# Performance work log

Measured on AMD Instinct MI355X. Metric: run time of the kernel, lower is better.

## Reference

```python
import jax, jax.numpy as jnp
import numpy as np

B, S, D, H, E, K = 8, 2048, 1024, 2048, 8, 2


def setup_inputs() -> dict:
    key = jax.random.key(0)
    k0, k1, k2, k3, k4 = jax.random.split(key, 5)
    x = jax.random.normal(k0, (B, S, D), jnp.float32)
    gate_w = jax.random.normal(k1, (E, D), jnp.float32) * (D ** -0.5)
    w1 = jax.random.normal(k2, (E, H, D), jnp.float32) * (D ** -0.5)
    w3 = jax.random.normal(k3, (E, H, D), jnp.float32) * (D ** -0.5)
    w2 = jax.random.normal(k4, (E, D, H), jnp.float32) * (H ** -0.5)
    return {"x": x, "gate_w": gate_w, "w1": w1, "w3": w3, "w2": w2, "k": K}


def reference(x, gate_w, w1, w3, w2, k):
    # Flatten tokens: [B, S, D] -> [T, D]
    x2 = x.reshape(-1, x.shape[-1])
    T = x2.shape[0]
    n_exp = gate_w.shape[0]
    # Gating: top-k logits, softmax over the k selected (in float32, cast back)
    logits = x2 @ gate_w.T                                  # [T, E]
    top_w, sel = jax.lax.top_k(logits, k)                   # [T, k] each
    top_w = jax.nn.softmax(top_w.astype(jnp.float32), axis=1).astype(x.dtype)
    # Dense combine weights [T, E]: zero for unselected experts (faithful to
    # the gather/scatter-add loop; topk indices are unique per token).
    cw = jnp.zeros((T, n_exp), x.dtype).at[jnp.arange(T)[:, None], sel].add(top_w)
    # Per-expert SwiGLU FFN, accumulated with combine weights.
    out = jnp.zeros_like(x2)
    for e in range(n_exp):  # fixed small structural loop over experts
        h = jax.nn.silu(x2 @ w1[e].T) * (x2 @ w3[e].T)      # [T, H]
        out = out + cw[:, e:e + 1] * (h @ w2[e].T)          # [T, D]
    return out.reshape(x.shape)
```

## Files before the change

kernel.cpp:

```cpp
#include <hip/hip_runtime.h>
#include <hip/hip_bf16.h>
#include <cstdint>


#define T_TOK 16384
#define DIM   1024
#define HID   2048
#define NEXP  8
#define MAX_TILES 264

typedef __bf16 bf16;
typedef bf16  bf16x8 __attribute__((ext_vector_type(8)));
typedef bf16  bf16x4 __attribute__((ext_vector_type(4)));
typedef float f32x16 __attribute__((ext_vector_type(16)));

__device__ __forceinline__ void async_cp16(const void* g, void* l) {
  __builtin_amdgcn_global_load_lds((const __attribute__((address_space(1))) void*)g,
                                   (__attribute__((address_space(3))) void*)l, 16, 0, 0);
}

__global__ __launch_bounds__(256) void zero_kernel(float4* __restrict__ out4, int n4,
                                                   int* __restrict__ ctrl) {
  const int i = blockIdx.x * 256 + threadIdx.x;
  if (i < n4) out4[i] = float4{0.f, 0.f, 0.f, 0.f};
  if (blockIdx.x == 0 && threadIdx.x < 64) ctrl[threadIdx.x] = 0;
}

__global__ __launch_bounds__(256) void cvt_kernel(const float* __restrict__ in,
                                                  bf16* __restrict__ out, int n4) {
  const int i = blockIdx.x * 256 + threadIdx.x;
  if (i < n4) {
    const float4 v = ((const float4*)in)[i];
    bf16x4 o;
    o[0] = (bf16)v.x; o[1] = (bf16)v.y; o[2] = (bf16)v.z; o[3] = (bf16)v.w;
    ((bf16x4*)out)[i] = o;
  }
}

__global__ __launch_bounds__(64) void gate_kernel(const float* __restrict__ x,
                                                  const float* __restrict__ gw,
                                                  int* __restrict__ sel,
                                                  float* __restrict__ selw) {
  const int t = blockIdx.x;
  const int lane = threadIdx.x;
  const float* xr = x + (size_t)t * DIM;
  float acc[NEXP];
#pragma unroll
  for (int e = 0; e < NEXP; e++) acc[e] = 0.f;
  for (int i = lane; i < DIM; i += 64) {
    const float xv = xr[i];
#pragma unroll
    for (int e = 0; e < NEXP; e++) acc[e] += xv * gw[e * DIM + i];
  }
#pragma unroll
  for (int e = 0; e < NEXP; e++) {
#pragma unroll
    for (int m = 1; m < 64; m <<= 1) acc[e] += __shfl_xor(acc[e], m);
  }
  if (lane == 0) {
    int e0 = 0; float l0 = acc[0];
#pragma unroll
    for (int e = 1; e < NEXP; e++) if (acc[e] > l0) { l0 = acc[e]; e0 = e; }
    int e1 = -1; float l1 = -3.4e38f;
#pragma unroll
    for (int e = 0; e < NEXP; e++) if (e != e0 && acc[e] > l1) { l1 = acc[e]; e1 = e; }
    const float ex = expf(l1 - l0);
    const float w0 = 1.f / (1.f + ex);
    sel[t * 2] = e0;  sel[t * 2 + 1] = e1;
    selw[t * 2] = w0; selw[t * 2 + 1] = 1.f - w0;
  }
}

__global__ __launch_bounds__(256) void count_kernel(const int* __restrict__ sel,
                                                    int* __restrict__ counts) {
  const int i = blockIdx.x * 256 + threadIdx.x;
  const int lane = threadIdx.x & 63;
  const int e = sel[i];
#pragma unroll
  for (int ee = 0; ee < NEXP; ee++) {
    const unsigned long long mask = __ballot(e == ee);
    if (e == ee) {
      const int leader = __ffsll(mask) - 1;
      if (lane == leader) atomicAdd(&counts[ee], __popcll(mask));
    }
  }
}

__global__ void tilemap_kernel(const int* __restrict__ counts, int* __restrict__ segoff,
                               int* __restrict__ tile_e, int* __restrict__ tile_m,
                               int* __restrict__ ntiles) {
  if (threadIdx.x == 0 && blockIdx.x == 0) {
    int off = 0, nt = 0;
    for (int e = 0; e < NEXP; e++) {
      segoff[e] = off;
      const int c = counts[e];
      for (int m = 0; m < c; m += 128) { tile_e[nt] = e; tile_m[nt] = m; nt++; }
      off += c;
    }
    segoff[NEXP] = off;
    ntiles[0] = nt;
  }
}

__global__ __launch_bounds__(256) void fill_kernel(const int* __restrict__ sel,
                                                   const float* __restrict__ selw,
                                                   const int* __restrict__ segoff,
                                                   int* __restrict__ fill,
                                                   int* __restrict__ tokl,
                                                   float* __restrict__ wl) {
  const int t = blockIdx.x * 256 + threadIdx.x;
  const int lane = threadIdx.x & 63;
#pragma unroll
  for (int s = 0; s < 2; s++) {
    const int e = sel[t * 2 + s];
    const float w = selw[t * 2 + s];
    for (int ee = 0; ee < NEXP; ee++) {
      const unsigned long long mask = __ballot(e == ee);
      if (e == ee) {
        const int leader = __ffsll(mask) - 1;
        const int cnt = __popcll(mask);
        int base = 0;
        if (lane == leader) base = atomicAdd(&fill[ee], cnt);
        base = __shfl(base, leader);
        const int pos = base + __popcll(mask & ((1ull << lane) - 1ull));
        const int idx = segoff[ee] + pos;
        tokl[idx] = t;
        wl[idx] = w;
      }
    }
  }
}

__global__ __launch_bounds__(256) void gemm_act_kernel(
    const bf16* __restrict__ xb, const bf16* __restrict__ w1b, const bf16* __restrict__ w3b,
    const int* __restrict__ tokl, const int* __restrict__ counts, const int* __restrict__ segoff,
    const int* __restrict__ tile_e, const int* __restrict__ tile_m, const int* __restrict__ ntiles,
    bf16* __restrict__ act) {
  const int tile = blockIdx.y;
  if (tile >= *ntiles) return;
  const int e   = tile_e[tile];
  const int m0  = tile_m[tile];
  const int n0  = blockIdx.x * 64;
  const int Ne  = counts[e];
  const int seg = segoff[e];

  __shared__ bf16 As[128 * 64];
  __shared__ bf16 Bs1[64 * 64];
  __shared__ bf16 Bs3[64 * 64];

  const int tid = threadIdx.x;
  const int lane = tid & 63;
  const int wv = tid >> 6;
  const int sr = tid >> 3;
  const int scb = (tid & 7) ^ (sr & 7);

  const bf16* aptr[4];
#pragma unroll
  for (int i = 0; i < 4; i++) {
    int m = m0 + sr + 32 * i; if (m > Ne - 1) m = Ne - 1;
    aptr[i] = xb + (size_t)tokl[seg + m] * DIM + scb * 8;
  }
  const bf16 *b1p[2], *b3p[2];
#pragma unroll
  for (int i = 0; i < 2; i++) {
    const int n = n0 + sr + 32 * i;
    b1p[i] = w1b + ((size_t)e * HID + n) * DIM + scb * 8;
    b3p[i] = w3b + ((size_t)e * HID + n) * DIM + scb * 8;
  }

  f32x16 acc1[2], acc3[2];
#pragma unroll
  for (int i = 0; i < 2; i++)
#pragma unroll
    for (int j = 0; j < 16; j++) { acc1[i][j] = 0.f; acc3[i][j] = 0.f; }

  const int lwm = (wv & 1) * 64;
  const int lwn = (wv >> 1) * 32;
  const int l31 = lane & 31;
  const int lhi = lane >> 5;
  const int l7  = l31 & 7;

  for (int k0 = 0; k0 < DIM; k0 += 64) {
#pragma unroll
    for (int i = 0; i < 4; i++)
      async_cp16(aptr[i] + k0, (char*)As + i * 4096 + tid * 16);
#pragma unroll
    for (int i = 0; i < 2; i++) {
      async_cp16(b1p[i] + k0, (char*)Bs1 + i * 4096 + tid * 16);
      async_cp16(b3p[i] + k0, (char*)Bs3 + i * 4096 + tid * 16);
    }
    __syncthreads();
#pragma unroll
    for (int ks = 0; ks < 4; ks++) {
      const int swz = (((ks * 2 + lhi) ^ l7) * 8);
      bf16x8 a0 = *(const bf16x8*)(As + (lwm + l31) * 64 + swz);
      bf16x8 a1 = *(const bf16x8*)(As + (lwm + 32 + l31) * 64 + swz);
      bf16x8 b1 = *(const bf16x8*)(Bs1 + (lwn + l31) * 64 + swz);
      bf16x8 b3 = *(const bf16x8*)(Bs3 + (lwn + l31) * 64 + swz);
      acc1[0] = __builtin_amdgcn_mfma_f32_32x32x16_bf16(a0, b1, acc1[0], 0, 0, 0);
      acc3[0] = __builtin_amdgcn_mfma_f32_32x32x16_bf16(a0, b3, acc3[0], 0, 0, 0);
      acc1[1] = __builtin_amdgcn_mfma_f32_32x32x16_bf16(a1, b1, acc1[1], 0, 0, 0);
      acc3[1] = __builtin_amdgcn_mfma_f32_32x32x16_bf16(a1, b3, acc3[1], 0, 0, 0);
    }
    __syncthreads();
  }

#pragma unroll
  for (int ms = 0; ms < 2; ms++) {
#pragma unroll
    for (int r = 0; r < 16; r++) {
      const int row = lwm + 32 * ms + (r & 3) + 8 * (r >> 2) + 4 * lhi;
      const int m = m0 + row;
      if (m < Ne) {
        const float h1 = acc1[ms][r];
        const float h3 = acc3[ms][r];
        const float sv = h1 / (1.f + __expf(-h1)) * h3;
        act[(size_t)(seg + m) * HID + (n0 + lwn + l31)] = (bf16)sv;
      }
    }
  }
}

__global__ __launch_bounds__(256) void gemm_out_kernel(
    const bf16* __restrict__ act, const bf16* __restrict__ w2b,
    const int* __restrict__ tokl, const float* __restrict__ wl,
    const int* __restrict__ counts, const int* __restrict__ segoff,
    const int* __restrict__ tile_e, const int* __restrict__ tile_m, const int* __restrict__ ntiles,
    float* __restrict__ out) {
  const int tile = blockIdx.y;
  if (tile >= *ntiles) return;
  const int e   = tile_e[tile];
  const int m0  = tile_m[tile];
  const int n0  = blockIdx.x * 128;
  const int Ne  = counts[e];
  const int seg = segoff[e];

  __shared__ bf16 As[128 * 64];
  __shared__ bf16 Bs[128 * 64];
  __shared__ int   sh_tok[128];
  __shared__ float sh_w[128];

  const int tid = threadIdx.x;
  const int lane = tid & 63;
  const int wv = tid >> 6;
  const int sr = tid >> 3;
  const int scb = (tid & 7) ^ (sr & 7);

  if (tid < 128) {
    const int m = m0 + tid;
    if (m < Ne) { sh_tok[tid] = tokl[seg + m]; sh_w[tid] = wl[seg + m]; }
    else        { sh_tok[tid] = -1;            sh_w[tid] = 0.f; }
  }

  const bf16* aptr[4];
#pragma unroll
  for (int i = 0; i < 4; i++) {
    int m = m0 + sr + 32 * i; if (m > Ne - 1) m = Ne - 1;
    aptr[i] = act + (size_t)(seg + m) * HID + scb * 8;
  }
  const bf16* bptr[4];
#pragma unroll
  for (int i = 0; i < 4; i++) {
    const int d = n0 + sr + 32 * i;
    bptr[i] = w2b + ((size_t)e * DIM + d) * HID + scb * 8;
  }

  f32x16 acc[4];
#pragma unroll
  for (int i = 0; i < 4; i++)
#pragma unroll
    for (int j = 0; j < 16; j++) acc[i][j] = 0.f;

  const int lwm = (wv & 1) * 64;
  const int lwn = (wv >> 1) * 64;
  const int l31 = lane & 31;
  const int lhi = lane >> 5;
  const int l7  = l31 & 7;

  for (int k0 = 0; k0 < HID; k0 += 64) {
#pragma unroll
    for (int i = 0; i < 4; i++)
      async_cp16(aptr[i] + k0, (char*)As + i * 4096 + tid * 16);
#pragma unroll
    for (int i = 0; i < 4; i++)
      async_cp16(bptr[i] + k0, (char*)Bs + i * 4096 + tid * 16);
    __syncthreads();
#pragma unroll
    for (int ks = 0; ks < 4; ks++) {
      const int swz = (((ks * 2 + lhi) ^ l7) * 8);
      bf16x8 a0 = *(const bf16x8*)(As + (lwm + l31) * 64 + swz);
      bf16x8 a1 = *(const bf16x8*)(As + (lwm + 32 + l31) * 64 + swz);
      bf16x8 b0 = *(const bf16x8*)(Bs + (lwn + l31) * 64 + swz);
      bf16x8 b1 = *(const bf16x8*)(Bs + (lwn + 32 + l31) * 64 + swz);
      acc[0] = __builtin_amdgcn_mfma_f32_32x32x16_bf16(a0, b0, acc[0], 0, 0, 0);
      acc[1] = __builtin_amdgcn_mfma_f32_32x32x16_bf16(a0, b1, acc[1], 0, 0, 0);
      acc[2] = __builtin_amdgcn_mfma_f32_32x32x16_bf16(a1, b0, acc[2], 0, 0, 0);
      acc[3] = __builtin_amdgcn_mfma_f32_32x32x16_bf16(a1, b1, acc[3], 0, 0, 0);
    }
    __syncthreads();
  }

#pragma unroll
  for (int mi = 0; mi < 2; mi++) {
#pragma unroll
    for (int ni = 0; ni < 2; ni++) {
#pragma unroll
      for (int r = 0; r < 16; r++) {
        const int row = lwm + 32 * mi + (r & 3) + 8 * (r >> 2) + 4 * lhi;
        const int tok = sh_tok[row];
        if (tok >= 0) {
          const int col = n0 + lwn + 32 * ni + l31;
          atomicAdd(&out[(size_t)tok * DIM + col], sh_w[row] * acc[mi * 2 + ni][r]);
        }
      }
    }
  }
}

extern "C" void kernel_launch(void* const* d_in, const int* in_sizes, int n_in,
                              void* d_out, int out_size, void* d_ws, size_t ws_size,
                              hipStream_t stream) {
  const float* x  = (const float*)d_in[0];
  const float* gw = (const float*)d_in[1];
  const float* w1 = (const float*)d_in[2];
  const float* w3 = (const float*)d_in[3];
  const float* w2 = (const float*)d_in[4];
  float* out = (float*)d_out;

  char* ws = (char*)d_ws;
  size_t off = 0;
  auto alloc = [&](size_t bytes) -> char* {
    char* p = ws + off; off += (bytes + 255) & ~(size_t)255; return p;
  };

  int* ctrl = (int*)alloc(4096);
  int* counts = ctrl;
  int* fill   = ctrl + 8;
  int* segoff = ctrl + 16;
  int* ntiles = ctrl + 32;
  int* tile_e = ctrl + 64;
  int* tile_m = ctrl + 512;
  int*   sel  = (int*)alloc((size_t)T_TOK * 2 * 4);
  float* selw = (float*)alloc((size_t)T_TOK * 2 * 4);
  int*   tokl = (int*)alloc((size_t)2 * T_TOK * 4);
  float* wl   = (float*)alloc((size_t)2 * T_TOK * 4);

  bf16* act  = (bf16*)alloc((size_t)2 * T_TOK * HID * 2);
  bf16* w1b  = (bf16*)alloc((size_t)NEXP * HID * DIM * 2);
  bf16* w3b  = (bf16*)alloc((size_t)NEXP * HID * DIM * 2);
  bf16* xb   = (bf16*)alloc((size_t)T_TOK * DIM * 2);
  bf16* w2b  = xb;
  (void)ws_size; (void)in_sizes; (void)n_in; (void)out_size;

  zero_kernel<<<T_TOK * DIM / 4 / 256, 256, 0, stream>>>((float4*)out, T_TOK * DIM / 4, ctrl);

  cvt_kernel<<<16384, 256, 0, stream>>>(x,  xb,  T_TOK * DIM / 4);
  cvt_kernel<<<16384, 256, 0, stream>>>(w1, w1b, NEXP * HID * DIM / 4);
  cvt_kernel<<<16384, 256, 0, stream>>>(w3, w3b, NEXP * HID * DIM / 4);

  gate_kernel<<<T_TOK, 64, 0, stream>>>(x, gw, sel, selw);
  count_kernel<<<2 * T_TOK / 256, 256, 0, stream>>>(sel, counts);
  tilemap_kernel<<<1, 64, 0, stream>>>(counts, segoff, tile_e, tile_m, ntiles);
  fill_kernel<<<T_TOK / 256, 256, 0, stream>>>(sel, selw, segoff, fill, tokl, wl);

  gemm_act_kernel<<<dim3(HID / 64, MAX_TILES), 256, 0, stream>>>(
      xb, w1b, w3b, tokl, counts, segoff, tile_e, tile_m, ntiles, act);

  cvt_kernel<<<16384, 256, 0, stream>>>(w2, w2b, NEXP * DIM * HID / 4);

  gemm_out_kernel<<<dim3(DIM / 128, MAX_TILES), 256, 0, stream>>>(
      act, w2b, tokl, wl, counts, segoff, tile_e, tile_m, ntiles, out);
}
```

Baseline: 1.036 ms.

## Enlarge GEMM tiles and replace atomic scatter-add with per-slot stores plus combine

Result: slower. 1.196 ms (+15.4%).

```diff
diff --git a/kernel.cpp b/kernel.cpp
--- a/kernel.cpp
+++ b/kernel.cpp
@@ -10,8 +10,10 @@
 #define MAX_TILES 264
 
 typedef __bf16 bf16;
+typedef _Float16 f16;
 typedef bf16  bf16x8 __attribute__((ext_vector_type(8)));
 typedef bf16  bf16x4 __attribute__((ext_vector_type(4)));
+typedef f16   f16x4  __attribute__((ext_vector_type(4)));
 typedef float f32x16 __attribute__((ext_vector_type(16)));
 
 __device__ __forceinline__ void async_cp16(const void* g, void* l) {
@@ -19,11 +21,8 @@
                                    (__attribute__((address_space(3))) void*)l, 16, 0, 0);
 }
 
-__global__ __launch_bounds__(256) void zero_kernel(float4* __restrict__ out4, int n4,
-                                                   int* __restrict__ ctrl) {
-  const int i = blockIdx.x * 256 + threadIdx.x;
-  if (i < n4) out4[i] = float4{0.f, 0.f, 0.f, 0.f};
-  if (blockIdx.x == 0 && threadIdx.x < 64) ctrl[threadIdx.x] = 0;
+__global__ void zero_ctrl_kernel(int* __restrict__ ctrl) {
+  if (threadIdx.x < 64) ctrl[threadIdx.x] = 0;
 }
 
 __global__ __launch_bounds__(256) void cvt_kernel(const float* __restrict__ in,
@@ -103,17 +102,14 @@
 }
 
 __global__ __launch_bounds__(256) void fill_kernel(const int* __restrict__ sel,
-                                                   const float* __restrict__ selw,
                                                    const int* __restrict__ segoff,
                                                    int* __restrict__ fill,
-                                                   int* __restrict__ tokl,
-                                                   float* __restrict__ wl) {
+                                                   int* __restrict__ tokl) {
   const int t = blockIdx.x * 256 + threadIdx.x;
   const int lane = threadIdx.x & 63;
 #pragma unroll
   for (int s = 0; s < 2; s++) {
     const int e = sel[t * 2 + s];
-    const float w = selw[t * 2 + s];
     for (int ee = 0; ee < NEXP; ee++) {
       const unsigned long long mask = __ballot(e == ee);
       if (e == ee) {
@@ -123,9 +119,7 @@
         if (lane == leader) base = atomicAdd(&fill[ee], cnt);
         base = __shfl(base, leader);
         const int pos = base + __popcll(mask & ((1ull << lane) - 1ull));
-        const int idx = segoff[ee] + pos;
-        tokl[idx] = t;
-        wl[idx] = w;
+        tokl[segoff[ee] + pos] = t | (s << 20);
       }
     }
   }
@@ -140,13 +134,13 @@
   if (tile >= *ntiles) return;
   const int e   = tile_e[tile];
   const int m0  = tile_m[tile];
-  const int n0  = blockIdx.x * 64;
+  const int n0  = blockIdx.x * 128;
   const int Ne  = counts[e];
   const int seg = segoff[e];
 
   __shared__ bf16 As[128 * 64];
-  __shared__ bf16 Bs1[64 * 64];
-  __shared__ bf16 Bs3[64 * 64];
+  __shared__ bf16 Bs1[128 * 64];
+  __shared__ bf16 Bs3[128 * 64];
 
   const int tid = threadIdx.x;
   const int lane = tid & 63;
@@ -158,24 +152,26 @@
 #pragma unroll
   for (int i = 0; i < 4; i++) {
     int m = m0 + sr + 32 * i; if (m > Ne - 1) m = Ne - 1;
-    aptr[i] = xb + (size_t)tokl[seg + m] * DIM + scb * 8;
-  }
-  const bf16 *b1p[2], *b3p[2];
-#pragma unroll
-  for (int i = 0; i < 2; i++) {
+    aptr[i] = xb + (size_t)(tokl[seg + m] & 0xFFFFF) * DIM + scb * 8;
+  }
+  const bf16 *b1p[4], *b3p[4];
+#pragma unroll
+  for (int i = 0; i < 4; i++) {
     const int n = n0 + sr + 32 * i;
     b1p[i] = w1b + ((size_t)e * HID + n) * DIM + scb * 8;
     b3p[i] = w3b + ((size_t)e * HID + n) * DIM + scb * 8;
   }
 
-  f32x16 acc1[2], acc3[2];
+  f32x16 acc1[2][2], acc3[2][2];
 #pragma unroll
   for (int i = 0; i < 2; i++)
 #pragma unroll
-    for (int j = 0; j < 16; j++) { acc1[i][j] = 0.f; acc3[i][j] = 0.f; }
+    for (int j = 0; j < 2; j++)
+#pragma unroll
+      for (int r = 0; r < 16; r++) { acc1[i][j][r] = 0.f; acc3[i][j][r] = 0.f; }
 
   const int lwm = (wv & 1) * 64;
-  const int lwn = (wv >> 1) * 32;
+  const int lwn = (wv >> 1) * 64;
   const int l31 = lane & 31;
   const int lhi = lane >> 5;
   const int l7  = l31 & 7;
@@ -185,22 +181,29 @@
     for (int i = 0; i < 4; i++)
       async_cp16(aptr[i] + k0, (char*)As + i * 4096 + tid * 16);
 #pragma unroll
-    for (int i = 0; i < 2; i++) {
+    for (int i = 0; i < 4; i++)
       async_cp16(b1p[i] + k0, (char*)Bs1 + i * 4096 + tid * 16);
+#pragma unroll
+    for (int i = 0; i < 4; i++)
       async_cp16(b3p[i] + k0, (char*)Bs3 + i * 4096 + tid * 16);
-    }
     __syncthreads();
 #pragma unroll
     for (int ks = 0; ks < 4; ks++) {
       const int swz = (((ks * 2 + lhi) ^ l7) * 8);
-      bf16x8 a0 = *(const bf16x8*)(As + (lwm + l31) * 64 + swz);
-      bf16x8 a1 = *(const bf16x8*)(As + (lwm + 32 + l31) * 64 + swz);
-      bf16x8 b1 = *(const bf16x8*)(Bs1 + (lwn + l31) * 64 + swz);
-      bf16x8 b3 = *(const bf16x8*)(Bs3 + (lwn + l31) * 64 + swz);
-      acc1[0] = __builtin_amdgcn_mfma_f32_32x32x16_bf16(a0, b1, acc1[0], 0, 0, 0);
-      acc3[0] = __builtin_amdgcn_mfma_f32_32x32x16_bf16(a0, b3, acc3[0], 0, 0, 0);
-      acc1[1] = __builtin_amdgcn_mfma_f32_32x32x16_bf16(a1, b1, acc1[1], 0, 0, 0);
-      acc3[1] = __builtin_amdgcn_mfma_f32_32x32x16_bf16(a1, b3, acc3[1], 0, 0, 0);
+      bf16x8 a0  = *(const bf16x8*)(As  + (lwm + l31) * 64 + swz);
+      bf16x8 a1  = *(const bf16x8*)(As  + (lwm + 32 + l31) * 64 + swz);
+      bf16x8 b10 = *(const bf16x8*)(Bs1 + (lwn + l31) * 64 + swz);
+      bf16x8 b11 = *(const bf16x8*)(Bs1 + (lwn + 32 + l31) * 64 + swz);
+      bf16x8 b30 = *(const bf16x8*)(Bs3 + (lwn + l31) * 64 + swz);
+      bf16x8 b31 = *(const bf16x8*)(Bs3 + (lwn + 32 + l31) * 64 + swz);
+      acc1[0][0] = __builtin_amdgcn_mfma_f32_32x32x16_bf16(a0, b10, acc1[0][0], 0, 0, 0);
+      acc1[0][1] = __builtin_amdgcn_mfma_f32_32x32x16_bf16(a0, b11, acc1[0][1], 0, 0, 0);
+      acc1[1][0] = __builtin_amdgcn_mfma_f32_32x32x16_bf16(a1, b10, acc1[1][0], 0, 0, 0);
+      acc1[1][1] = __builtin_amdgcn_mfma_f32_32x32x16_bf16(a1, b11, acc1[1][1], 0, 0, 0);
+      acc3[0][0] = __builtin_amdgcn_mfma_f32_32x32x16_bf16(a0, b30, acc3[0][0], 0, 0, 0);
+      acc3[0][1] = __builtin_amdgcn_mfma_f32_32x32x16_bf16(a0, b31, acc3[0][1], 0, 0, 0);
+      acc3[1][0] = __builtin_amdgcn_mfma_f32_32x32x16_bf16(a1, b30, acc3[1][0], 0, 0, 0);
+      acc3[1][1] = __builtin_amdgcn_mfma_f32_32x32x16_bf16(a1, b31, acc3[1][1], 0, 0, 0);
     }
     __syncthreads();
   }
@@ -212,10 +215,13 @@
       const int row = lwm + 32 * ms + (r & 3) + 8 * (r >> 2) + 4 * lhi;
       const int m = m0 + row;
       if (m < Ne) {
-        const float h1 = acc1[ms][r];
-        const float h3 = acc3[ms][r];
-        const float sv = h1 / (1.f + __expf(-h1)) * h3;
-        act[(size_t)(seg + m) * HID + (n0 + lwn + l31)] = (bf16)sv;
+        bf16* arow = act + (size_t)(seg + m) * HID + n0 + lwn;
+#pragma unroll
+        for (int ns = 0; ns < 2; ns++) {
+          const float h1 = acc1[ms][ns][r];
+          const float h3 = acc3[ms][ns][r];
+          arow[32 * ns + l31] = (bf16)(h1 / (1.f + __expf(-h1)) * h3);
+        }
       }
     }
   }
@@ -223,22 +229,21 @@
 
 __global__ __launch_bounds__(256) void gemm_out_kernel(
     const bf16* __restrict__ act, const bf16* __restrict__ w2b,
-    const int* __restrict__ tokl, const float* __restrict__ wl,
+    const int* __restrict__ tokl,
     const int* __restrict__ counts, const int* __restrict__ segoff,
     const int* __restrict__ tile_e, const int* __restrict__ tile_m, const int* __restrict__ ntiles,
-    float* __restrict__ out) {
+    f16* __restrict__ y) {
   const int tile = blockIdx.y;
   if (tile >= *ntiles) return;
   const int e   = tile_e[tile];
   const int m0  = tile_m[tile];
-  const int n0  = blockIdx.x * 128;
+  const int n0  = blockIdx.x * 256;
   const int Ne  = counts[e];
   const int seg = segoff[e];
 
   __shared__ bf16 As[128 * 64];
-  __shared__ bf16 Bs[128 * 64];
-  __shared__ int   sh_tok[128];
-  __shared__ float sh_w[128];
+  __shared__ bf16 Bs[256 * 64];
+  __shared__ int  sh_tok[128];
 
   const int tid = threadIdx.x;
   const int lane = tid & 63;
@@ -248,8 +253,7 @@
 
   if (tid < 128) {
     const int m = m0 + tid;
-    if (m < Ne) { sh_tok[tid] = tokl[seg + m]; sh_w[tid] = wl[seg + m]; }
-    else        { sh_tok[tid] = -1;            sh_w[tid] = 0.f; }
+    sh_tok[tid] = (m < Ne) ? tokl[seg + m] : -1;
   }
 
   const bf16* aptr[4];
@@ -258,21 +262,23 @@
     int m = m0 + sr + 32 * i; if (m > Ne - 1) m = Ne - 1;
     aptr[i] = act + (size_t)(seg + m) * HID + scb * 8;
   }
-  const bf16* bptr[4];
-#pragma unroll
-  for (int i = 0; i < 4; i++) {
+  const bf16* bptr[8];
+#pragma unroll
+  for (int i = 0; i < 8; i++) {
     const int d = n0 + sr + 32 * i;
     bptr[i] = w2b + ((size_t)e * DIM + d) * HID + scb * 8;
   }
 
-  f32x16 acc[4];
-#pragma unroll
-  for (int i = 0; i < 4; i++)
-#pragma unroll
-    for (int j = 0; j < 16; j++) acc[i][j] = 0.f;
+  f32x16 acc[2][4];
+#pragma unroll
+  for (int i = 0; i < 2; i++)
+#pragma unroll
+    for (int j = 0; j < 4; j++)
+#pragma unroll
+      for (int r = 0; r < 16; r++) acc[i][j][r] = 0.f;
 
   const int lwm = (wv & 1) * 64;
-  const int lwn = (wv >> 1) * 64;
+  const int lwn = (wv >> 1) * 128;
   const int l31 = lane & 31;
   const int lhi = lane >> 5;
   const int l7  = l31 & 7;
@@ -282,7 +288,7 @@
     for (int i = 0; i < 4; i++)
       async_cp16(aptr[i] + k0, (char*)As + i * 4096 + tid * 16);
 #pragma unroll
-    for (int i = 0; i < 4; i++)
+    for (int i = 0; i < 8; i++)
       async_cp16(bptr[i] + k0, (char*)Bs + i * 4096 + tid * 16);
     __syncthreads();
 #pragma unroll
@@ -292,10 +298,16 @@
       bf16x8 a1 = *(const bf16x8*)(As + (lwm + 32 + l31) * 64 + swz);
       bf16x8 b0 = *(const bf16x8*)(Bs + (lwn + l31) * 64 + swz);
       bf16x8 b1 = *(const bf16x8*)(Bs + (lwn + 32 + l31) * 64 + swz);
-      acc[0] = __builtin_amdgcn_mfma_f32_32x32x16_bf16(a0, b0, acc[0], 0, 0, 0);
-      acc[1] = __builtin_amdgcn_mfma_f32_32x32x16_bf16(a0, b1, acc[1], 0, 0, 0);
-      acc[2] = __builtin_amdgcn_mfma_f32_32x32x16_bf16(a1, b0, acc[2], 0, 0, 0);
-      acc[3] = __builtin_amdgcn_mfma_f32_32x32x16_bf16(a1, b1, acc[3], 0, 0, 0);
+      bf16x8 b2 = *(const bf16x8*)(Bs + (lwn + 64 + l31) * 64 + swz);
+      bf16x8 b3 = *(const bf16x8*)(Bs + (lwn + 96 + l31) * 64 + swz);
+      acc[0][0] = __builtin_amdgcn_mfma_f32_32x32x16_bf16(a0, b0, acc[0][0], 0, 0, 0);
+      acc[0][1] = __builtin_amdgcn_mfma_f32_32x32x16_bf16(a0, b1, acc[0][1], 0, 0, 0);
+      acc[0][2] = __builtin_amdgcn_mfma_f32_32x32x16_bf16(a0, b2, acc[0][2], 0, 0, 0);
+      acc[0][3] = __builtin_amdgcn_mfma_f32_32x32x16_bf16(a0, b3, acc[0][3], 0, 0, 0);
+      acc[1][0] = __builtin_amdgcn_mfma_f32_32x32x16_bf16(a1, b0, acc[1][0], 0, 0, 0);
+      acc[1][1] = __builtin_amdgcn_mfma_f32_32x32x16_bf16(a1, b1, acc[1][1], 0, 0, 0);
+      acc[1][2] = __builtin_amdgcn_mfma_f32_32x32x16_bf16(a1, b2, acc[1][2], 0, 0, 0);
+      acc[1][3] = __builtin_amdgcn_mfma_f32_32x32x16_bf16(a1, b3, acc[1][3], 0, 0, 0);
     }
     __syncthreads();
   }
@@ -303,18 +315,36 @@
 #pragma unroll
   for (int mi = 0; mi < 2; mi++) {
 #pragma unroll
-    for (int ni = 0; ni < 2; ni++) {
-#pragma unroll
-      for (int r = 0; r < 16; r++) {
-        const int row = lwm + 32 * mi + (r & 3) + 8 * (r >> 2) + 4 * lhi;
-        const int tok = sh_tok[row];
-        if (tok >= 0) {
-          const int col = n0 + lwn + 32 * ni + l31;
-          atomicAdd(&out[(size_t)tok * DIM + col], sh_w[row] * acc[mi * 2 + ni][r]);
-        }
+    for (int r = 0; r < 16; r++) {
+      const int row = lwm + 32 * mi + (r & 3) + 8 * (r >> 2) + 4 * lhi;
+      const int raw = sh_tok[row];
+      if (raw >= 0) {
+        const int s = raw >> 20;
+        const int t = raw & 0xFFFFF;
+        f16* yrow = y + ((size_t)s * T_TOK + t) * DIM + n0 + lwn;
+#pragma unroll
+        for (int ni = 0; ni < 4; ni++)
+          yrow[32 * ni + l31] = (f16)acc[mi][ni][r];
       }
     }
   }
+}
+
+__global__ __launch_bounds__(256) void combine_kernel(const f16* __restrict__ y,
+                                                      const float* __restrict__ selw,
+                                                      float* __restrict__ out) {
+  const int t = blockIdx.x;
+  const int d4 = threadIdx.x;
+  const float w0 = selw[2 * t];
+  const float w1 = selw[2 * t + 1];
+  const f16x4 a = ((const f16x4*)y)[(size_t)t * 256 + d4];
+  const f16x4 b = ((const f16x4*)y)[((size_t)T_TOK + t) * 256 + d4];
+  float4 o;
+  o.x = w0 * (float)a[0] + w1 * (float)b[0];
+  o.y = w0 * (float)a[1] + w1 * (float)b[1];
+  o.z = w0 * (float)a[2] + w1 * (float)b[2];
+  o.w = w0 * (float)a[3] + w1 * (float)b[3];
+  ((float4*)out)[(size_t)t * 256 + d4] = o;
 }
 
 extern "C" void kernel_launch(void* const* d_in, const int* in_sizes, int n_in,
@@ -343,16 +373,16 @@
   int*   sel  = (int*)alloc((size_t)T_TOK * 2 * 4);
   float* selw = (float*)alloc((size_t)T_TOK * 2 * 4);
   int*   tokl = (int*)alloc((size_t)2 * T_TOK * 4);
-  float* wl   = (float*)alloc((size_t)2 * T_TOK * 4);
 
   bf16* act  = (bf16*)alloc((size_t)2 * T_TOK * HID * 2);
   bf16* w1b  = (bf16*)alloc((size_t)NEXP * HID * DIM * 2);
   bf16* w3b  = (bf16*)alloc((size_t)NEXP * HID * DIM * 2);
   bf16* xb   = (bf16*)alloc((size_t)T_TOK * DIM * 2);
   bf16* w2b  = xb;
+  f16*  y    = (f16*)w1b;
   (void)ws_size; (void)in_sizes; (void)n_in; (void)out_size;
 
-  zero_kernel<<<T_TOK * DIM / 4 / 256, 256, 0, stream>>>((float4*)out, T_TOK * DIM / 4, ctrl);
+  zero_ctrl_kernel<<<1, 64, 0, stream>>>(ctrl);
 
   cvt_kernel<<<16384, 256, 0, stream>>>(x,  xb,  T_TOK * DIM / 4);
   cvt_kernel<<<16384, 256, 0, stream>>>(w1, w1b, NEXP * HID * DIM / 4);
@@ -361,13 +391,15 @@
   gate_kernel<<<T_TOK, 64, 0, stream>>>(x, gw, sel, selw);
   count_kernel<<<2 * T_TOK / 256, 256, 0, stream>>>(sel, counts);
   tilemap_kernel<<<1, 64, 0, stream>>>(counts, segoff, tile_e, tile_m, ntiles);
-  fill_kernel<<<T_TOK / 256, 256, 0, stream>>>(sel, selw, segoff, fill, tokl, wl);
-
-  gemm_act_kernel<<<dim3(HID / 64, MAX_TILES), 256, 0, stream>>>(
+  fill_kernel<<<T_TOK / 256, 256, 0, stream>>>(sel, segoff, fill, tokl);
+
+  gemm_act_kernel<<<dim3(HID / 128, MAX_TILES), 256, 0, stream>>>(
       xb, w1b, w3b, tokl, counts, segoff, tile_e, tile_m, ntiles, act);
 
   cvt_kernel<<<16384, 256, 0, stream>>>(w2, w2b, NEXP * DIM * HID / 4);
 
-  gemm_out_kernel<<<dim3(DIM / 128, MAX_TILES), 256, 0, stream>>>(
-      act, w2b, tokl, wl, counts, segoff, tile_e, tile_m, ntiles, out);
-}
+  gemm_out_kernel<<<dim3(DIM / 256, MAX_TILES), 256, 0, stream>>>(
+      act, w2b, tokl, counts, segoff, tile_e, tile_m, ntiles, y);
+
+  combine_kernel<<<T_TOK, 256, 0, stream>>>(y, selw, out);
+}
```
